# Performance work log

Measured on AMD Instinct MI355X. Metric: run time of the kernel, lower is better.

Reference implementation:

```python
import jax, jax.numpy as jnp
import numpy as np

N_ENT = 40000
D = 128
B = 1024
EPS = 1e-7  # BCE clamp for numerical stability (torch clamps logs internally)


def _cdist_euclidean(a, e):
    # a: [B, D], e: [N, D] -> [B, N] via GEMM-based squared-distance expansion
    sq = jnp.sum(a * a, axis=1)[:, None] + jnp.sum(e * e, axis=1)[None, :] - 2.0 * (a @ e.T)
    return jnp.sqrt(jnp.maximum(sq, 0.0))


def _cdist_manhattan(a, e):
    # Sequential over batch rows to avoid materializing [B, N, D]
    return jax.lax.map(lambda row: jnp.sum(jnp.abs(row[None, :] - e), axis=1), a)


def _branch_loss(c, ent, t_idx, l1_flag, positive):
    dist = _cdist_manhattan(c, ent) if l1_flag else _cdist_euclidean(c, ent)
    # original Python double-loop: dist[i][j] = 1/dist[i][j] * 100
    scaled = 100.0 / jnp.maximum(dist, 1e-12)
    pred = jnp.clip(jax.nn.sigmoid(scaled), EPS, 1.0 - EPS)
    if positive:
        y = jnp.zeros_like(pred).at[jnp.arange(pred.shape[0]), t_idx].set(1.0)
        bce = y * jnp.log(pred) + (1.0 - y) * jnp.log(1.0 - pred)
    else:
        # negative branch writes 0 into an all-zeros target -> y == 0
        bce = jnp.log(1.0 - pred)
    return -jnp.mean(bce)


def setup_inputs() -> dict:
    key = jax.random.key(0)
    ks = jax.random.split(key, 7)
    return {
        "pos_h_batch": jax.random.randint(ks[0], (B,), 0, N_ENT),
        "pos_t_batch": jax.random.randint(ks[1], (B,), 0, N_ENT),
        "neg_h_batch": jax.random.randint(ks[2], (B,), 0, N_ENT),
        "neg_t_batch": jax.random.randint(ks[3], (B,), 0, N_ENT),
        "rseq_pos": jax.random.normal(ks[4], (B, D), jnp.float32),
        "rseq_neg": jax.random.normal(ks[5], (B, D), jnp.float32),
        "ent_embeddings": jax.random.normal(ks[6], (N_ENT, D), jnp.float32),
        "L1_flag": 0,
    }


def reference(pos_h_batch, pos_t_batch, neg_h_batch, neg_t_batch, rseq_pos, rseq_neg, ent_embeddings, L1_flag):
    l1 = bool(L1_flag)
    # positive branch
    c_t_pos = ent_embeddings[pos_h_batch] + rseq_pos
    loss1 = _branch_loss(c_t_pos, ent_embeddings, pos_t_batch, l1, positive=True)
    # negative branch (neg_t_batch only feeds an unused c_h_e in the original)
    c_t_neg = ent_embeddings[neg_h_batch] + rseq_neg
    loss2 = _branch_loss(c_t_neg, ent_embeddings, None, l1, positive=False)
    return loss1 + loss2
```

## Files before the change

### kernel.cpp

```cpp
#include <hip/hip_runtime.h>
#include <cstdint>
#include <cstddef>

#define N_ENT 40000
#define DDIM  128
#define BSZ   1024
#define NJT   313
#define NPART (16 * NJT)
#define CH    5
#define NGRID 1024

#define AS1 __attribute__((address_space(1)))
#define AS3 __attribute__((address_space(3)))

typedef short s16x8 __attribute__((ext_vector_type(8)));
typedef float f32x4 __attribute__((ext_vector_type(4)));

#define OFF_PART  0
#define OFF_TPART 20480
#define OFF_ENORM 24576
#define OFF_CNORM 184576
#define OFF_CBF   192768
#define OFF_EBF   717056

#define S_CLAMP 15.9423847f
#define U_CLAMP 0.159423847f
#define LP_MAX (-1.1920929e-7f)

__device__ __forceinline__ unsigned short f2bf(float f) {
  uint32_t u = __float_as_uint(f);
  u += 0x7fffu + ((u >> 16) & 1u);
  return (unsigned short)(u >> 16);
}

__global__ __launch_bounds__(256) void prep_k(const float* __restrict__ ent,
                                              const int* __restrict__ pos_h,
                                              const int* __restrict__ pos_t,
                                              const int* __restrict__ neg_h,
                                              const float* __restrict__ rpos,
                                              const float* __restrict__ rneg,
                                              const int* __restrict__ l1_flag,
                                              unsigned short* __restrict__ ent_bf,
                                              float* __restrict__ enorm,
                                              unsigned short* __restrict__ c_bf,
                                              float* __restrict__ cnorm,
                                              float* __restrict__ tpart) {
  const int lane = threadIdx.x & 63, wv = threadIdx.x >> 6;
  const int ih = lane >> 5, il = lane & 31;
  const int blk = blockIdx.x;
  if (blk < 5000) {
    int row = blk * 8 + wv * 2 + ih;
    float4 v = reinterpret_cast<const float4*>(ent + (size_t)row * DDIM)[il];
    ushort4 h4; h4.x = f2bf(v.x); h4.y = f2bf(v.y); h4.z = f2bf(v.z); h4.w = f2bf(v.w);
    reinterpret_cast<ushort4*>(ent_bf + (size_t)row * DDIM)[il] = h4;
    float sq = fmaf(v.x, v.x, fmaf(v.y, v.y, fmaf(v.z, v.z, v.w * v.w)));
    #pragma unroll
    for (int m = 1; m <= 16; m <<= 1) sq += __shfl_xor(sq, m);
    if (il == 0) enorm[row] = sq;
  } else {
    int row = (blk - 5000) * 8 + wv * 2 + ih;
    int br = row >> 10, i = row & 1023;
    int h = br ? neg_h[i] : pos_h[i];
    const float* rs = br ? rneg : rpos;
    float4 e  = reinterpret_cast<const float4*>(ent + (size_t)h * DDIM)[il];
    float4 rv = reinterpret_cast<const float4*>(rs + (size_t)i * DDIM)[il];
    float c0 = e.x + rv.x, c1 = e.y + rv.y, c2 = e.z + rv.z, c3 = e.w + rv.w;
    ushort4 h4; h4.x = f2bf(c0); h4.y = f2bf(c1); h4.z = f2bf(c2); h4.w = f2bf(c3);
    reinterpret_cast<ushort4*>(c_bf + (size_t)row * DDIM)[il] = h4;
    float sq = fmaf(c0, c0, fmaf(c1, c1, fmaf(c2, c2, c3 * c3)));
    #pragma unroll
    for (int m = 1; m <= 16; m <<= 1) sq += __shfl_xor(sq, m);
    if (il == 0) cnorm[row] = sq;
    if (br == 0) {
      int t = pos_t[i];
      float4 et = reinterpret_cast<const float4*>(ent + (size_t)t * DDIM)[il];
      float d0 = c0 - et.x, d1 = c1 - et.y, d2v = c2 - et.z, d3 = c3 - et.w;
      float d2 = fmaf(d0, d0, fmaf(d1, d1, fmaf(d2v, d2v, d3 * d3)));
      float m1 = fabsf(d0) + fabsf(d1) + fabsf(d2v) + fabsf(d3);
      #pragma unroll
      for (int m = 1; m <= 16; m <<= 1) { d2 += __shfl_xor(d2, m); m1 += __shfl_xor(m1, m); }
      if (il == 0) {
        float s = (*l1_flag) ? (100.f / fmaxf(m1, 1e-12f))
                             : (100.f * rsqrtf(fmaxf(d2, 0.f)));
        float x  = __expf(-s);
        float L  = log1pf(x);
        float Bt = fminf(-L, LP_MAX);
        float Ap = fmaxf(-s, -S_CLAMP);
        tpart[i] = Bt - Ap;
      }
    }
  }
}

__global__ __launch_bounds__(256, 2) void main_k(const unsigned short* __restrict__ c_bf,
                                                 const unsigned short* __restrict__ ent_bf,
                                                 const float* __restrict__ cnorm,
                                                 const float* __restrict__ enorm,
                                                 const int* __restrict__ l1_flag,
                                                 const int* __restrict__ pos_h,
                                                 const int* __restrict__ neg_h,
                                                 const float* __restrict__ rpos,
                                                 const float* __restrict__ rneg,
                                                 const float* __restrict__ ent_f32,
                                                 float* __restrict__ partials) {
  __shared__ unsigned short smem[2][128 * 128];
  __shared__ float s4[2][4];
  const int id = blockIdx.x;
  const int c8 = id & 7;
  const int q  = id >> 3;
  const int mm = q & 15;
  const int gg = q >> 4;
  const int gp = c8 * 8 + gg;
  const int jtB = gp * CH;
  if (jtB >= NJT) return;
  const int nt = (jtB + CH <= NJT) ? CH : (NJT - jtB);
  const int branch = mm & 1;
  const int i0 = (mm >> 1) * 128;
  const int tid = threadIdx.x, lane = tid & 63, wv = tid >> 6;
  const int wm = wv >> 1, wn = wv & 1;
  const int r15 = lane & 15, quad = lane >> 4;

#define STAGE(par_, j0_) do {                                                  \
    _Pragma("unroll")                                                          \
    for (int i_ = 0; i_ < 8; ++i_) {                                           \
      int g_  = i_ * 256 + tid;          \
      int r_  = g_ >> 4;                                                       \
      int c_  = (g_ & 15) ^ (r_ & 15);                                         \
      int jr_ = (j0_) + r_; if (jr_ >= N_ENT) jr_ = N_ENT - 1;                 \
      const unsigned short* src_ = ent_bf + (size_t)jr_ * DDIM + c_ * 8;       \
      __builtin_amdgcn_global_load_lds((const AS1 void*)src_,                  \
          (AS3 void*)(&smem[par_][g_ * 8]), 16, 0, 0);                         \
    }                                                                          \
  } while (0)

  STAGE(0, jtB * 128);

  const unsigned short* Abase = c_bf + ((size_t)(branch << 10) + i0) * DDIM;
  s16x8 avk[4][4];
  #pragma unroll
  for (int tm = 0; tm < 4; ++tm) {
    const unsigned short* ar = Abase + (size_t)(wm * 64 + tm * 16 + r15) * DDIM + quad * 8;
    #pragma unroll
    for (int kc = 0; kc < 4; ++kc)
      avk[kc][tm] = *reinterpret_cast<const s16x8*>(ar + kc * 32);
  }

  float cnv[16];
  #pragma unroll
  for (int tm = 0; tm < 4; ++tm)
    #pragma unroll
    for (int r = 0; r < 4; ++r)
      cnv[tm * 4 + r] = cnorm[(branch << 10) + i0 + wm * 64 + tm * 16 + quad * 4 + r];

  float en[4];
  #pragma unroll
  for (int tn = 0; tn < 4; ++tn) {
    int jg = jtB * 128 + wn * 64 + tn * 16 + r15;
    en[tn] = enorm[jg < N_ENT ? jg : N_ENT - 1];
  }

  const int l1 = *l1_flag;
  const f32x4 zf = {0.f, 0.f, 0.f, 0.f};

  __syncthreads();

  #pragma unroll 1
  for (int t = 0; t < nt; ++t) {
    const int jt  = jtB + t;
    const int j0  = jt * 128;
    const int par = t & 1;
    const bool haveNext = (t + 1) < nt;

    if (haveNext) STAGE(par ^ 1, j0 + 128);

    float enx[4];
    if (haveNext) {
      #pragma unroll
      for (int tn = 0; tn < 4; ++tn) {
        int jg = j0 + 128 + wn * 64 + tn * 16 + r15;
        enx[tn] = enorm[jg < N_ENT ? jg : N_ENT - 1];
      }
    }

    f32x4 acc[4][4];
    #pragma unroll
    for (int a = 0; a < 4; ++a)
      #pragma unroll
      for (int b = 0; b < 4; ++b) acc[a][b] = zf;

    #pragma unroll
    for (int kc = 0; kc < 4; ++kc) {
      s16x8 bv[4];
      #pragma unroll
      for (int tn = 0; tn < 4; ++tn) {
        int R  = wn * 64 + tn * 16 + r15;
        int cs = (kc * 4 + quad) ^ r15;
        bv[tn] = *reinterpret_cast<const s16x8*>(&smem[par][R * 128 + cs * 8]);
      }
      #pragma unroll
      for (int tm = 0; tm < 4; ++tm)
        #pragma unroll
        for (int tn = 0; tn < 4; ++tn)
          acc[tm][tn] = __builtin_amdgcn_mfma_f32_16x16x32_bf16(avk[kc][tm], bv[tn], acc[tm][tn], 0, 0, 0);
    }

    const bool full = (j0 + 128) <= N_ENT;
    float ls0 = 0.f, ls1 = 0.f, ls2 = 0.f, ls3 = 0.f;
    if (!l1) {
      #pragma unroll
      for (int tm = 0; tm < 4; ++tm) {
        if (full) {
          #pragma unroll
          for (int tn = 0; tn < 4; ++tn) {
            float e0 = en[tn];
            float u0 = rsqrtf(fmaf(-2.f, acc[tm][tn][0], cnv[tm * 4 + 0] + e0));
            float u1 = rsqrtf(fmaf(-2.f, acc[tm][tn][1], cnv[tm * 4 + 1] + e0));
            float u2 = rsqrtf(fmaf(-2.f, acc[tm][tn][2], cnv[tm * 4 + 2] + e0));
            float u3 = rsqrtf(fmaf(-2.f, acc[tm][tn][3], cnv[tm * 4 + 3] + e0));
            ls0 += fminf(u0, U_CLAMP);
            ls1 += fminf(u1, U_CLAMP);
            ls2 += fminf(u2, U_CLAMP);
            ls3 += fminf(u3, U_CLAMP);
          }
        } else {
          #pragma unroll
          for (int tn = 0; tn < 4; ++tn) {
            int jg = j0 + wn * 64 + tn * 16 + r15;
            if (jg < N_ENT) {
              float e0 = en[tn];
              ls0 += fminf(rsqrtf(fmaf(-2.f, acc[tm][tn][0], cnv[tm * 4 + 0] + e0)), U_CLAMP);
              ls1 += fminf(rsqrtf(fmaf(-2.f, acc[tm][tn][1], cnv[tm * 4 + 1] + e0)), U_CLAMP);
              ls2 += fminf(rsqrtf(fmaf(-2.f, acc[tm][tn][2], cnv[tm * 4 + 2] + e0)), U_CLAMP);
              ls3 += fminf(rsqrtf(fmaf(-2.f, acc[tm][tn][3], cnv[tm * 4 + 3] + e0)), U_CLAMP);
            }
          }
        }
      }
    } else {
      const float* rs = branch ? rneg : rpos;
      const int*   hb = branch ? neg_h : pos_h;
      #pragma unroll 1
      for (int tm = 0; tm < 4; ++tm) {
        #pragma unroll 1
        for (int r = 0; r < 4; ++r) {
          int bi = i0 + wm * 64 + tm * 16 + quad * 4 + r;
          int hh = hb[bi];
          #pragma unroll 1
          for (int tn = 0; tn < 4; ++tn) {
            int jg = j0 + wn * 64 + tn * 16 + r15;
            if (jg < N_ENT) {
              const float* cp1 = ent_f32 + (size_t)hh * DDIM;
              const float* cp2 = rs + (size_t)bi * DDIM;
              const float* ep  = ent_f32 + (size_t)jg * DDIM;
              float man = 0.f;
              #pragma unroll 1
              for (int d = 0; d < DDIM; ++d) man += fabsf(cp1[d] + cp2[d] - ep[d]);
              float s = 100.f / fmaxf(man, 1e-12f);
              ls0 += 0.01f * fminf(s, S_CLAMP);
            }
          }
        }
      }
    }
    float lsum = (ls0 + ls1) + (ls2 + ls3);

    #pragma unroll
    for (int m = 32; m; m >>= 1) lsum += __shfl_xor(lsum, m);
    if (lane == 0) s4[par][wv] = lsum;

    if (haveNext) {
      #pragma unroll
      for (int tn = 0; tn < 4; ++tn) en[tn] = enx[tn];
    }

    __syncthreads();
    if (tid == 0)
      partials[jt * 16 + mm] = s4[par][0] + s4[par][1] + s4[par][2] + s4[par][3];
  }
#undef STAGE
}

__global__ __launch_bounds__(1024) void finalize_k(const float* __restrict__ partials,
                                                   const float* __restrict__ tpart,
                                                   float* __restrict__ out) {
  const int tid = threadIdx.x, lane = tid & 63, wv = tid >> 6;
  const double inv = 1.0 / ((double)BSZ * (double)N_ENT);
  double v = 0.0;
  for (int i = tid; i < NPART; i += 1024) v += (double)partials[i] * (100.0 * inv);
  v += (double)tpart[tid] * (-inv);
  #pragma unroll
  for (int m = 32; m; m >>= 1) v += __shfl_xor(v, m);
  __shared__ double sd[16];
  if (lane == 0) sd[wv] = v;
  __syncthreads();
  if (wv == 0) {
    double t = (lane < 16) ? sd[lane] : 0.0;
    #pragma unroll
    for (int m = 8; m; m >>= 1) t += __shfl_xor(t, m);
    if (lane == 0) out[0] = (float)t;
  }
}

extern "C" void kernel_launch(void* const* d_in, const int* in_sizes, int n_in,
                              void* d_out, int out_size, void* d_ws, size_t ws_size,
                              hipStream_t stream) {
  const int*   pos_h = (const int*)d_in[0];
  const int*   pos_t = (const int*)d_in[1];
  const int*   neg_h = (const int*)d_in[2];
  const float* rpos  = (const float*)d_in[4];
  const float* rneg  = (const float*)d_in[5];
  const float* ent   = (const float*)d_in[6];
  const int*   l1    = (const int*)d_in[7];

  char* ws = (char*)d_ws;
  float*          partials = (float*)(ws + OFF_PART);
  float*          tpart    = (float*)(ws + OFF_TPART);
  float*          enorm    = (float*)(ws + OFF_ENORM);
  float*          cnorm    = (float*)(ws + OFF_CNORM);
  unsigned short* c_bf     = (unsigned short*)(ws + OFF_CBF);
  unsigned short* ent_bf   = (unsigned short*)(ws + OFF_EBF);

  prep_k<<<5256, 256, 0, stream>>>(ent, pos_h, pos_t, neg_h, rpos, rneg, l1,
                                   ent_bf, enorm, c_bf, cnorm, tpart);

  main_k<<<NGRID, 256, 0, stream>>>(c_bf, ent_bf, cnorm, enorm, l1,
                                    pos_h, neg_h, rpos, rneg, ent, partials);

  finalize_k<<<1, 1024, 0, stream>>>(partials, tpart, (float*)d_out);
}
```

Before: 133.8 us.

## Load B tiles directly into registers instead of LDS and reduce once per block

Removes the shared-memory double buffer and its global_load_lds staging. Each wave now loads its entity-tile fragments straight from global memory into registers and software-pipelines them across k-chunks against the MFMAs. Per-tile block reductions and __syncthreads are replaced by a single reduction per block, which writes one partial per block id, and finalize reads exactly one partial per thread. The trade-off is that waves no longer share B data through LDS, so global and L2 traffic per wave goes up, and the launch bounds hint for 2 blocks per CU is dropped.

```diff
diff --git a/kernel.cpp b/kernel.cpp
--- a/kernel.cpp
+++ b/kernel.cpp
@@ -6,12 +6,8 @@
 #define DDIM  128
 #define BSZ   1024
 #define NJT   313
-#define NPART (16 * NJT)
 #define CH    5
 #define NGRID 1024
-
-#define AS1 __attribute__((address_space(1)))
-#define AS3 __attribute__((address_space(3)))
 
 typedef short s16x8 __attribute__((ext_vector_type(8)));
 typedef float f32x4 __attribute__((ext_vector_type(4)));
@@ -92,19 +88,18 @@
   }
 }
 
-__global__ __launch_bounds__(256, 2) void main_k(const unsigned short* __restrict__ c_bf,
-                                                 const unsigned short* __restrict__ ent_bf,
-                                                 const float* __restrict__ cnorm,
-                                                 const float* __restrict__ enorm,
-                                                 const int* __restrict__ l1_flag,
-                                                 const int* __restrict__ pos_h,
-                                                 const int* __restrict__ neg_h,
-                                                 const float* __restrict__ rpos,
-                                                 const float* __restrict__ rneg,
-                                                 const float* __restrict__ ent_f32,
-                                                 float* __restrict__ partials) {
-  __shared__ unsigned short smem[2][128 * 128];
-  __shared__ float s4[2][4];
+__global__ __launch_bounds__(256) void main_k(const unsigned short* __restrict__ c_bf,
+                                              const unsigned short* __restrict__ ent_bf,
+                                              const float* __restrict__ cnorm,
+                                              const float* __restrict__ enorm,
+                                              const int* __restrict__ l1_flag,
+                                              const int* __restrict__ pos_h,
+                                              const int* __restrict__ neg_h,
+                                              const float* __restrict__ rpos,
+                                              const float* __restrict__ rneg,
+                                              const float* __restrict__ ent_f32,
+                                              float* __restrict__ partials) {
+  __shared__ float s4[4];
   const int id = blockIdx.x;
   const int c8 = id & 7;
   const int q  = id >> 3;
@@ -112,28 +107,26 @@
   const int gg = q >> 4;
   const int gp = c8 * 8 + gg;
   const int jtB = gp * CH;
-  if (jtB >= NJT) return;
+  const int tid = threadIdx.x, lane = tid & 63, wv = tid >> 6;
+  if (jtB >= NJT) {
+    if (tid == 0) partials[id] = 0.f;
+    return;
+  }
   const int nt = (jtB + CH <= NJT) ? CH : (NJT - jtB);
   const int branch = mm & 1;
   const int i0 = (mm >> 1) * 128;
-  const int tid = threadIdx.x, lane = tid & 63, wv = tid >> 6;
   const int wm = wv >> 1, wn = wv & 1;
   const int r15 = lane & 15, quad = lane >> 4;
 
-#define STAGE(par_, j0_) do {                                                  \
+#define LOADB(dst_, j0_, kc_) do {                                             \
     _Pragma("unroll")                                                          \
-    for (int i_ = 0; i_ < 8; ++i_) {                                           \
-      int g_  = i_ * 256 + tid;          \
-      int r_  = g_ >> 4;                                                       \
-      int c_  = (g_ & 15) ^ (r_ & 15);                                         \
-      int jr_ = (j0_) + r_; if (jr_ >= N_ENT) jr_ = N_ENT - 1;                 \
-      const unsigned short* src_ = ent_bf + (size_t)jr_ * DDIM + c_ * 8;       \
-      __builtin_amdgcn_global_load_lds((const AS1 void*)src_,                  \
-          (AS3 void*)(&smem[par_][g_ * 8]), 16, 0, 0);                         \
+    for (int tn_ = 0; tn_ < 4; ++tn_) {                                        \
+      int jg_ = (j0_) + wn * 64 + tn_ * 16 + r15;                              \
+      if (jg_ >= N_ENT) jg_ = N_ENT - 1;                                       \
+      dst_[tn_] = *reinterpret_cast<const s16x8*>(                             \
+          ent_bf + (size_t)jg_ * DDIM + ((kc_) * 4 + quad) * 8);               \
     }                                                                          \
   } while (0)
-
-  STAGE(0, jtB * 128);
 
   const unsigned short* Abase = c_bf + ((size_t)(branch << 10) + i0) * DDIM;
   s16x8 avk[4][4];
@@ -162,16 +155,46 @@
   const int l1 = *l1_flag;
   const f32x4 zf = {0.f, 0.f, 0.f, 0.f};
 
-  __syncthreads();
+  s16x8 bv0[4], bv1[4];
+  LOADB(bv0, jtB * 128, 0);
+
+  float ls0 = 0.f, ls1 = 0.f, ls2 = 0.f, ls3 = 0.f;
 
   #pragma unroll 1
   for (int t = 0; t < nt; ++t) {
-    const int jt  = jtB + t;
-    const int j0  = jt * 128;
-    const int par = t & 1;
+    const int j0 = (jtB + t) * 128;
     const bool haveNext = (t + 1) < nt;
 
-    if (haveNext) STAGE(par ^ 1, j0 + 128);
+    f32x4 acc[4][4];
+    #pragma unroll
+    for (int a = 0; a < 4; ++a)
+      #pragma unroll
+      for (int b = 0; b < 4; ++b) acc[a][b] = zf;
+
+    LOADB(bv1, j0, 1);
+    #pragma unroll
+    for (int tm = 0; tm < 4; ++tm)
+      #pragma unroll
+      for (int tn = 0; tn < 4; ++tn)
+        acc[tm][tn] = __builtin_amdgcn_mfma_f32_16x16x32_bf16(avk[0][tm], bv0[tn], acc[tm][tn], 0, 0, 0);
+    LOADB(bv0, j0, 2);
+    #pragma unroll
+    for (int tm = 0; tm < 4; ++tm)
+      #pragma unroll
+      for (int tn = 0; tn < 4; ++tn)
+        acc[tm][tn] = __builtin_amdgcn_mfma_f32_16x16x32_bf16(avk[1][tm], bv1[tn], acc[tm][tn], 0, 0, 0);
+    LOADB(bv1, j0, 3);
+    #pragma unroll
+    for (int tm = 0; tm < 4; ++tm)
+      #pragma unroll
+      for (int tn = 0; tn < 4; ++tn)
+        acc[tm][tn] = __builtin_amdgcn_mfma_f32_16x16x32_bf16(avk[2][tm], bv0[tn], acc[tm][tn], 0, 0, 0);
+    if (haveNext) LOADB(bv0, j0 + 128, 0);
+    #pragma unroll
+    for (int tm = 0; tm < 4; ++tm)
+      #pragma unroll
+      for (int tn = 0; tn < 4; ++tn)
+        acc[tm][tn] = __builtin_amdgcn_mfma_f32_16x16x32_bf16(avk[3][tm], bv1[tn], acc[tm][tn], 0, 0, 0);
 
     float enx[4];
     if (haveNext) {
@@ -182,30 +205,7 @@
       }
     }
 
-    f32x4 acc[4][4];
-    #pragma unroll
-    for (int a = 0; a < 4; ++a)
-      #pragma unroll
-      for (int b = 0; b < 4; ++b) acc[a][b] = zf;
-
-    #pragma unroll
-    for (int kc = 0; kc < 4; ++kc) {
-      s16x8 bv[4];
-      #pragma unroll
-      for (int tn = 0; tn < 4; ++tn) {
-        int R  = wn * 64 + tn * 16 + r15;
-        int cs = (kc * 4 + quad) ^ r15;
-        bv[tn] = *reinterpret_cast<const s16x8*>(&smem[par][R * 128 + cs * 8]);
-      }
-      #pragma unroll
-      for (int tm = 0; tm < 4; ++tm)
-        #pragma unroll
-        for (int tn = 0; tn < 4; ++tn)
-          acc[tm][tn] = __builtin_amdgcn_mfma_f32_16x16x32_bf16(avk[kc][tm], bv[tn], acc[tm][tn], 0, 0, 0);
-    }
-
     const bool full = (j0 + 128) <= N_ENT;
-    float ls0 = 0.f, ls1 = 0.f, ls2 = 0.f, ls3 = 0.f;
     if (!l1) {
       #pragma unroll
       for (int tm = 0; tm < 4; ++tm) {
@@ -262,22 +262,21 @@
         }
       }
     }
-    float lsum = (ls0 + ls1) + (ls2 + ls3);
-
-    #pragma unroll
-    for (int m = 32; m; m >>= 1) lsum += __shfl_xor(lsum, m);
-    if (lane == 0) s4[par][wv] = lsum;
 
     if (haveNext) {
       #pragma unroll
       for (int tn = 0; tn < 4; ++tn) en[tn] = enx[tn];
     }
-
-    __syncthreads();
-    if (tid == 0)
-      partials[jt * 16 + mm] = s4[par][0] + s4[par][1] + s4[par][2] + s4[par][3];
-  }
-#undef STAGE
+  }
+
+  float lsum = (ls0 + ls1) + (ls2 + ls3);
+  #pragma unroll
+  for (int m = 32; m; m >>= 1) lsum += __shfl_xor(lsum, m);
+  if (lane == 0) s4[wv] = lsum;
+  __syncthreads();
+  if (tid == 0)
+    partials[id] = (s4[0] + s4[1]) + (s4[2] + s4[3]);
+#undef LOADB
 }
 
 __global__ __launch_bounds__(1024) void finalize_k(const float* __restrict__ partials,
@@ -285,9 +284,7 @@
                                                    float* __restrict__ out) {
   const int tid = threadIdx.x, lane = tid & 63, wv = tid >> 6;
   const double inv = 1.0 / ((double)BSZ * (double)N_ENT);
-  double v = 0.0;
-  for (int i = tid; i < NPART; i += 1024) v += (double)partials[i] * (100.0 * inv);
-  v += (double)tpart[tid] * (-inv);
+  double v = (double)partials[tid] * (100.0 * inv) + (double)tpart[tid] * (-inv);
   #pragma unroll
   for (int m = 32; m; m >>= 1) v += __shfl_xor(v, m);
   __shared__ double sd[16];
```

After: 143.6 us. 7.3% more time.

## Process both branches per block to reuse staged entity tiles, halve grid

Applied to the files above, without the earlier changes.

Each block now computes the positive and negative branches against the same staged entity tile, so each 128-row entity tile is loaded into LDS once per row-block pair instead of twice. The grid halves to 512 blocks, per-tile partial writes are replaced by one accumulated partial per block, and finalize reads one partial per block. In exchange the A fragments and row norms are reloaded from global each tile and branch instead of staying in registers, and the occupancy hint of 2 is dropped. With fewer blocks, parallelism across CUs is reduced.

```diff
diff --git a/kernel.cpp b/kernel.cpp
--- a/kernel.cpp
+++ b/kernel.cpp
@@ -6,9 +6,8 @@
 #define DDIM  128
 #define BSZ   1024
 #define NJT   313
-#define NPART (16 * NJT)
 #define CH    5
-#define NGRID 1024
+#define NGRID 512
 
 #define AS1 __attribute__((address_space(1)))
 #define AS3 __attribute__((address_space(3)))
@@ -92,31 +91,33 @@
   }
 }
 
-__global__ __launch_bounds__(256, 2) void main_k(const unsigned short* __restrict__ c_bf,
-                                                 const unsigned short* __restrict__ ent_bf,
-                                                 const float* __restrict__ cnorm,
-                                                 const float* __restrict__ enorm,
-                                                 const int* __restrict__ l1_flag,
-                                                 const int* __restrict__ pos_h,
-                                                 const int* __restrict__ neg_h,
-                                                 const float* __restrict__ rpos,
-                                                 const float* __restrict__ rneg,
-                                                 const float* __restrict__ ent_f32,
-                                                 float* __restrict__ partials) {
+__global__ __launch_bounds__(256) void main_k(const unsigned short* __restrict__ c_bf,
+                                              const unsigned short* __restrict__ ent_bf,
+                                              const float* __restrict__ cnorm,
+                                              const float* __restrict__ enorm,
+                                              const int* __restrict__ l1_flag,
+                                              const int* __restrict__ pos_h,
+                                              const int* __restrict__ neg_h,
+                                              const float* __restrict__ rpos,
+                                              const float* __restrict__ rneg,
+                                              const float* __restrict__ ent_f32,
+                                              float* __restrict__ partials) {
   __shared__ unsigned short smem[2][128 * 128];
-  __shared__ float s4[2][4];
+  __shared__ float s4[4];
   const int id = blockIdx.x;
   const int c8 = id & 7;
   const int q  = id >> 3;
-  const int mm = q & 15;
-  const int gg = q >> 4;
+  const int p  = q & 7;
+  const int gg = q >> 3;
   const int gp = c8 * 8 + gg;
   const int jtB = gp * CH;
-  if (jtB >= NJT) return;
+  const int tid = threadIdx.x, lane = tid & 63, wv = tid >> 6;
+  if (jtB >= NJT) {
+    if (tid == 0) partials[id] = 0.f;
+    return;
+  }
   const int nt = (jtB + CH <= NJT) ? CH : (NJT - jtB);
-  const int branch = mm & 1;
-  const int i0 = (mm >> 1) * 128;
-  const int tid = threadIdx.x, lane = tid & 63, wv = tid >> 6;
+  const int i0 = p * 128;
   const int wm = wv >> 1, wn = wv & 1;
   const int r15 = lane & 15, quad = lane >> 4;
 
@@ -135,148 +136,136 @@
 
   STAGE(0, jtB * 128);
 
-  const unsigned short* Abase = c_bf + ((size_t)(branch << 10) + i0) * DDIM;
-  s16x8 avk[4][4];
-  #pragma unroll
-  for (int tm = 0; tm < 4; ++tm) {
-    const unsigned short* ar = Abase + (size_t)(wm * 64 + tm * 16 + r15) * DDIM + quad * 8;
-    #pragma unroll
-    for (int kc = 0; kc < 4; ++kc)
-      avk[kc][tm] = *reinterpret_cast<const s16x8*>(ar + kc * 32);
-  }
-
-  float cnv[16];
-  #pragma unroll
-  for (int tm = 0; tm < 4; ++tm)
-    #pragma unroll
-    for (int r = 0; r < 4; ++r)
-      cnv[tm * 4 + r] = cnorm[(branch << 10) + i0 + wm * 64 + tm * 16 + quad * 4 + r];
-
-  float en[4];
-  #pragma unroll
-  for (int tn = 0; tn < 4; ++tn) {
-    int jg = jtB * 128 + wn * 64 + tn * 16 + r15;
-    en[tn] = enorm[jg < N_ENT ? jg : N_ENT - 1];
-  }
-
   const int l1 = *l1_flag;
   const f32x4 zf = {0.f, 0.f, 0.f, 0.f};
+  float ls0 = 0.f, ls1 = 0.f, ls2 = 0.f, ls3 = 0.f;
 
   __syncthreads();
 
   #pragma unroll 1
   for (int t = 0; t < nt; ++t) {
-    const int jt  = jtB + t;
-    const int j0  = jt * 128;
+    const int j0  = (jtB + t) * 128;
     const int par = t & 1;
     const bool haveNext = (t + 1) < nt;
 
     if (haveNext) STAGE(par ^ 1, j0 + 128);
 
-    float enx[4];
-    if (haveNext) {
-      #pragma unroll
-      for (int tn = 0; tn < 4; ++tn) {
-        int jg = j0 + 128 + wn * 64 + tn * 16 + r15;
-        enx[tn] = enorm[jg < N_ENT ? jg : N_ENT - 1];
+    float en[4];
+    #pragma unroll
+    for (int tn = 0; tn < 4; ++tn) {
+      int jg = j0 + wn * 64 + tn * 16 + r15;
+      en[tn] = enorm[jg < N_ENT ? jg : N_ENT - 1];
+    }
+    const bool full = (j0 + 128) <= N_ENT;
+
+    #pragma unroll
+    for (int k = 0; k < 2; ++k) {
+      const unsigned short* Ab = c_bf + ((size_t)(k << 10) + i0) * DDIM;
+      s16x8 av[4][4];
+      #pragma unroll
+      for (int tm = 0; tm < 4; ++tm) {
+        const unsigned short* ar = Ab + (size_t)(wm * 64 + tm * 16 + r15) * DDIM + quad * 8;
+        #pragma unroll
+        for (int kc = 0; kc < 4; ++kc)
+          av[kc][tm] = *reinterpret_cast<const s16x8*>(ar + kc * 32);
       }
-    }
-
-    f32x4 acc[4][4];
-    #pragma unroll
-    for (int a = 0; a < 4; ++a)
-      #pragma unroll
-      for (int b = 0; b < 4; ++b) acc[a][b] = zf;
-
-    #pragma unroll
-    for (int kc = 0; kc < 4; ++kc) {
-      s16x8 bv[4];
-      #pragma unroll
-      for (int tn = 0; tn < 4; ++tn) {
-        int R  = wn * 64 + tn * 16 + r15;
-        int cs = (kc * 4 + quad) ^ r15;
-        bv[tn] = *reinterpret_cast<const s16x8*>(&smem[par][R * 128 + cs * 8]);
+      float cnvA[16];
+      #pragma unroll
+      for (int tm = 0; tm < 4; ++tm)
+        #pragma unroll
+        for (int r = 0; r < 4; ++r)
+          cnvA[tm * 4 + r] = cnorm[(k << 10) + i0 + wm * 64 + tm * 16 + quad * 4 + r];
+
+      f32x4 acc[4][4];
+      #pragma unroll
+      for (int a = 0; a < 4; ++a)
+        #pragma unroll
+        for (int b = 0; b < 4; ++b) acc[a][b] = zf;
+
+      #pragma unroll
+      for (int kc = 0; kc < 4; ++kc) {
+        s16x8 bv[4];
+        #pragma unroll
+        for (int tn = 0; tn < 4; ++tn) {
+          int R  = wn * 64 + tn * 16 + r15;
+          int cs = (kc * 4 + quad) ^ r15;
+          bv[tn] = *reinterpret_cast<const s16x8*>(&smem[par][R * 128 + cs * 8]);
+        }
+        #pragma unroll
+        for (int tm = 0; tm < 4; ++tm)
+          #pragma unroll
+          for (int tn = 0; tn < 4; ++tn)
+            acc[tm][tn] = __builtin_amdgcn_mfma_f32_16x16x32_bf16(av[kc][tm], bv[tn], acc[tm][tn], 0, 0, 0);
       }
-      #pragma unroll
-      for (int tm = 0; tm < 4; ++tm)
-        #pragma unroll
-        for (int tn = 0; tn < 4; ++tn)
-          acc[tm][tn] = __builtin_amdgcn_mfma_f32_16x16x32_bf16(avk[kc][tm], bv[tn], acc[tm][tn], 0, 0, 0);
-    }
-
-    const bool full = (j0 + 128) <= N_ENT;
-    float ls0 = 0.f, ls1 = 0.f, ls2 = 0.f, ls3 = 0.f;
-    if (!l1) {
-      #pragma unroll
-      for (int tm = 0; tm < 4; ++tm) {
-        if (full) {
-          #pragma unroll
-          for (int tn = 0; tn < 4; ++tn) {
-            float e0 = en[tn];
-            float u0 = rsqrtf(fmaf(-2.f, acc[tm][tn][0], cnv[tm * 4 + 0] + e0));
-            float u1 = rsqrtf(fmaf(-2.f, acc[tm][tn][1], cnv[tm * 4 + 1] + e0));
-            float u2 = rsqrtf(fmaf(-2.f, acc[tm][tn][2], cnv[tm * 4 + 2] + e0));
-            float u3 = rsqrtf(fmaf(-2.f, acc[tm][tn][3], cnv[tm * 4 + 3] + e0));
-            ls0 += fminf(u0, U_CLAMP);
-            ls1 += fminf(u1, U_CLAMP);
-            ls2 += fminf(u2, U_CLAMP);
-            ls3 += fminf(u3, U_CLAMP);
-          }
-        } else {
-          #pragma unroll
-          for (int tn = 0; tn < 4; ++tn) {
-            int jg = j0 + wn * 64 + tn * 16 + r15;
-            if (jg < N_ENT) {
+
+      if (!l1) {
+        #pragma unroll
+        for (int tm = 0; tm < 4; ++tm) {
+          if (full) {
+            #pragma unroll
+            for (int tn = 0; tn < 4; ++tn) {
               float e0 = en[tn];
-              ls0 += fminf(rsqrtf(fmaf(-2.f, acc[tm][tn][0], cnv[tm * 4 + 0] + e0)), U_CLAMP);
-              ls1 += fminf(rsqrtf(fmaf(-2.f, acc[tm][tn][1], cnv[tm * 4 + 1] + e0)), U_CLAMP);
-              ls2 += fminf(rsqrtf(fmaf(-2.f, acc[tm][tn][2], cnv[tm * 4 + 2] + e0)), U_CLAMP);
-              ls3 += fminf(rsqrtf(fmaf(-2.f, acc[tm][tn][3], cnv[tm * 4 + 3] + e0)), U_CLAMP);
+              float u0 = rsqrtf(fmaf(-2.f, acc[tm][tn][0], cnvA[tm * 4 + 0] + e0));
+              float u1 = rsqrtf(fmaf(-2.f, acc[tm][tn][1], cnvA[tm * 4 + 1] + e0));
+              float u2 = rsqrtf(fmaf(-2.f, acc[tm][tn][2], cnvA[tm * 4 + 2] + e0));
+              float u3 = rsqrtf(fmaf(-2.f, acc[tm][tn][3], cnvA[tm * 4 + 3] + e0));
+              ls0 += fminf(u0, U_CLAMP);
+              ls1 += fminf(u1, U_CLAMP);
+              ls2 += fminf(u2, U_CLAMP);
+              ls3 += fminf(u3, U_CLAMP);
+            }
+          } else {
+            #pragma unroll
+            for (int tn = 0; tn < 4; ++tn) {
+              int jg = j0 + wn * 64 + tn * 16 + r15;
+              if (jg < N_ENT) {
+                float e0 = en[tn];
+                ls0 += fminf(rsqrtf(fmaf(-2.f, acc[tm][tn][0], cnvA[tm * 4 + 0] + e0)), U_CLAMP);
+                ls1 += fminf(rsqrtf(fmaf(-2.f, acc[tm][tn][1], cnvA[tm * 4 + 1] + e0)), U_CLAMP);
+                ls2 += fminf(rsqrtf(fmaf(-2.f, acc[tm][tn][2], cnvA[tm * 4 + 2] + e0)), U_CLAMP);
+                ls3 += fminf(rsqrtf(fmaf(-2.f, acc[tm][tn][3], cnvA[tm * 4 + 3] + e0)), U_CLAMP);
+              }
             }
           }
         }
-      }
-    } else {
-      const float* rs = branch ? rneg : rpos;
-      const int*   hb = branch ? neg_h : pos_h;
-      #pragma unroll 1
-      for (int tm = 0; tm < 4; ++tm) {
+      } else {
+        const float* rs = k ? rneg : rpos;
+        const int*   hb = k ? neg_h : pos_h;
         #pragma unroll 1
-        for (int r = 0; r < 4; ++r) {
-          int bi = i0 + wm * 64 + tm * 16 + quad * 4 + r;
-          int hh = hb[bi];
+        for (int tm = 0; tm < 4; ++tm) {
           #pragma unroll 1
-          for (int tn = 0; tn < 4; ++tn) {
-            int jg = j0 + wn * 64 + tn * 16 + r15;
-            if (jg < N_ENT) {
-              const float* cp1 = ent_f32 + (size_t)hh * DDIM;
-              const float* cp2 = rs + (size_t)bi * DDIM;
-              const float* ep  = ent_f32 + (size_t)jg * DDIM;
-              float man = 0.f;
-              #pragma unroll 1
-              for (int d = 0; d < DDIM; ++d) man += fabsf(cp1[d] + cp2[d] - ep[d]);
-              float s = 100.f / fmaxf(man, 1e-12f);
-              ls0 += 0.01f * fminf(s, S_CLAMP);
+          for (int r = 0; r < 4; ++r) {
+            int bi = i0 + wm * 64 + tm * 16 + quad * 4 + r;
+            int hh = hb[bi];
+            #pragma unroll 1
+            for (int tn = 0; tn < 4; ++tn) {
+              int jg = j0 + wn * 64 + tn * 16 + r15;
+              if (jg < N_ENT) {
+                const float* cp1 = ent_f32 + (size_t)hh * DDIM;
+                const float* cp2 = rs + (size_t)bi * DDIM;
+                const float* ep  = ent_f32 + (size_t)jg * DDIM;
+                float man = 0.f;
+                #pragma unroll 1
+                for (int d = 0; d < DDIM; ++d) man += fabsf(cp1[d] + cp2[d] - ep[d]);
+                float s = 100.f / fmaxf(man, 1e-12f);
+                ls0 += 0.01f * fminf(s, S_CLAMP);
+              }
             }
           }
         }
       }
     }
-    float lsum = (ls0 + ls1) + (ls2 + ls3);
-
-    #pragma unroll
-    for (int m = 32; m; m >>= 1) lsum += __shfl_xor(lsum, m);
-    if (lane == 0) s4[par][wv] = lsum;
-
-    if (haveNext) {
-      #pragma unroll
-      for (int tn = 0; tn < 4; ++tn) en[tn] = enx[tn];
-    }
 
     __syncthreads();
-    if (tid == 0)
-      partials[jt * 16 + mm] = s4[par][0] + s4[par][1] + s4[par][2] + s4[par][3];
   }
+
+  float lsum = (ls0 + ls1) + (ls2 + ls3);
+  #pragma unroll
+  for (int m = 32; m; m >>= 1) lsum += __shfl_xor(lsum, m);
+  if (lane == 0) s4[wv] = lsum;
+  __syncthreads();
+  if (tid == 0)
+    partials[id] = (s4[0] + s4[1]) + (s4[2] + s4[3]);
 #undef STAGE
 }
 
@@ -285,9 +274,8 @@
                                                    float* __restrict__ out) {
   const int tid = threadIdx.x, lane = tid & 63, wv = tid >> 6;
   const double inv = 1.0 / ((double)BSZ * (double)N_ENT);
-  double v = 0.0;
-  for (int i = tid; i < NPART; i += 1024) v += (double)partials[i] * (100.0 * inv);
-  v += (double)tpart[tid] * (-inv);
+  double v = (double)tpart[tid] * (-inv);
+  if (tid < NGRID) v += (double)partials[tid] * (100.0 * inv);
   #pragma unroll
   for (int m = 32; m; m >>= 1) v += __shfl_xor(v, m);
   __shared__ double sd[16];
```

Measured after the change: 143.9 us. 1.07x slower.
